# Optimization experiments

Hardware: AMD Instinct MI355X
Metric: run time of the kernel (lower is better)

The kernel has to match this reference:

```python
import jax, jax.numpy as jnp
import numpy as np

N = 400000   # nnum_t (tokens)
C = 256      # dim
H = 8        # num_heads
HD = C // H  # head_dim = 32
K = 32       # patch_size
D = 4        # dilation
BLOCK = K * D
NA = ((N + BLOCK - 1) // BLOCK) * BLOCK  # nnum_a (padded length)
SCALE = HD ** -0.5
INVALID = -1000.0


def setup_inputs() -> dict:
    key = jax.random.key(0)
    ks = jax.random.split(key, 8)
    data = jax.random.normal(ks[0], (N, C), dtype=jnp.float32)
    xyz = jax.random.uniform(ks[1], (N, 3), dtype=jnp.float32) * 1024.0
    depth_idx = jnp.sort(jax.random.randint(ks[2], (N,), 0, 8)).astype(jnp.int64)
    Wqkv = jax.random.normal(ks[3], (C, 3 * C), dtype=jnp.float32) * 0.02
    bqkv = jnp.zeros((3 * C,), dtype=jnp.float32)
    Wproj = jax.random.normal(ks[4], (C, C), dtype=jnp.float32) * 0.02
    bproj = jnp.zeros((C,), dtype=jnp.float32)
    freqs = jax.random.normal(ks[5], (H, HD // 2, 3), dtype=jnp.float32) * 0.02
    return {"data": data, "xyz": xyz, "depth_idx": depth_idx,
            "Wqkv": Wqkv, "bqkv": bqkv, "Wproj": Wproj, "bproj": bproj,
            "freqs": freqs}


def _rotate_half(x):
    x1, x2 = jnp.split(x, 2, axis=-1)
    return jnp.concatenate([-x2, x1], axis=-1)


def reference(data, xyz, depth_idx, Wqkv, bqkv, Wproj, bproj, freqs):
    # qkv projection: (N, 3C)
    qkv = data @ Wqkv + bqkv
    qkv = qkv.reshape(N, 3, H, HD)

    # mixed RoPE: per-head learnable frequencies over 3D positions
    theta = jnp.einsum('nd,hfd->nhf', xyz, freqs)          # (N, H, HD/2)
    emb = jnp.concatenate([theta, theta], axis=-1)         # (N, H, HD)
    cos, sin = jnp.cos(emb), jnp.sin(emb)
    q = qkv[:, 0] * cos + _rotate_half(qkv[:, 0]) * sin
    k = qkv[:, 1] * cos + _rotate_half(qkv[:, 1]) * sin
    v = qkv[:, 2]
    qkv = jnp.stack([q, k, v], axis=1).reshape(N, 3 * C)

    # patch_partition: pad tokens to nnum_a
    pad = NA - N
    qkv = jnp.pad(qkv, ((0, pad), (0, 0)))
    max_d = depth_idx.max()
    depth_p = jnp.pad(depth_idx, (0, pad), constant_values=0) 
    if pad > 0:
        depth_p = depth_p.at[N:].set(max_d + 1)

    # dilation reshuffle: (-1, K, D, 3C) -> (-1, D, K, 3C) -> (-1, K, 3C)
    qkv = qkv.reshape(-1, K, D, 3 * C).transpose(0, 2, 1, 3).reshape(-1, K, 3 * C)
    # split heads: (B, H, K, HD) each
    qkv = qkv.reshape(-1, K, 3, H, HD).transpose(2, 0, 3, 1, 4)
    q, k, v = qkv[0], qkv[1], qkv[2]

    # teacher-forcing mask from depth indices (dilated layout, cond='le')
    m = depth_p.reshape(-1, K, D).transpose(0, 2, 1).reshape(-1, K)  # (B, K)
    diff = m[:, :, None] - m[:, None, :]
    mask = jnp.where(diff < 0, INVALID, 0.0).astype(jnp.float32)     # (B, K, K)

    # windowed attention
    scores = jnp.einsum('bhqd,bhkd->bhqk', q, k) * SCALE + mask[:, None]
    attn = jax.nn.softmax(scores, axis=-1)
    out = jnp.einsum('bhqk,bhkd->bhqd', attn, v)           # (B, H, K, HD)
    out = out.transpose(0, 2, 1, 3).reshape(-1, C)

    # reverse dilation reshuffle and unpad
    out = out.reshape(-1, D, K, C).transpose(0, 2, 1, 3).reshape(-1, C)
    out = out[:N]

    # output projection (dropout is identity at p=0 / eval)
    return out @ Wproj + bproj
```

## Files before the change

kernel.cpp:

```cpp
#include <hip/hip_runtime.h>
#include <math.h>


typedef float  float4v __attribute__((ext_vector_type(4)));
typedef short  bf16x8  __attribute__((ext_vector_type(8)));
typedef unsigned short us4 __attribute__((ext_vector_type(4)));

#define SCALE_ 0.17677669529663687f
#define INV2PI 0.15915494309189535f

__device__ __forceinline__ unsigned short f2bf(float x) {
  union { float f; unsigned u; } v; v.f = x;
  unsigned r = v.u + 0x7FFFu + ((v.u >> 16) & 1u);
  return (unsigned short)(r >> 16);
}
__device__ __forceinline__ unsigned pack2bf(float lo, float hi) {
  return (unsigned)f2bf(lo) | ((unsigned)f2bf(hi) << 16);
}
__device__ __forceinline__ float4v mfma16(bf16x8 a, bf16x8 b, float4v c) {
  return __builtin_amdgcn_mfma_f32_16x16x32_bf16(a, b, c, 0, 0, 0);
}
__device__ __forceinline__ int swz(int off) {
  return off ^ (((off >> 9) & 7) << 4);
}

__global__ __launch_bounds__(256) void k_prep(const float* __restrict__ wqkv,
                                              const float* __restrict__ wproj,
                                              unsigned short* __restrict__ wq,
                                              unsigned short* __restrict__ wp) {
  int tid = blockIdx.x * 256 + threadIdx.x;
  if (tid < 768 * 256) {
    int co = tid >> 8, ci = tid & 255;
    wq[tid] = f2bf(wqkv[ci * 768 + co]);
  } else {
    int u = tid - 768 * 256;
    int co = u >> 8, cpos = u & 255;
    int h = cpos >> 5, ww = cpos & 31;
    int f = (ww & 1) ? 16 + (ww >> 1) : (ww >> 1);
    wp[u] = f2bf(wproj[(h * 32 + f) * 256 + co]);
  }
}

#define K1_LDS_BYTES 81920

__global__ __launch_bounds__(512, 4) void k_fused(
    const float* __restrict__ data, const float* __restrict__ xyz,
    const int* __restrict__ depth, const float* __restrict__ bqkv,
    const float* __restrict__ freqs, const unsigned short* __restrict__ wqkv_t,
    unsigned short* __restrict__ aout ) {
  extern __shared__ char smem[];
  const int b    = blockIdx.x;
  const int t    = threadIdx.x;
  const int lane = t & 63;
  const int w    = t >> 6;
  const int g    = lane >> 4;
  const int l15  = lane & 15;
  const int d    = w >> 1;
  const int half = w & 1;

  if (t < 128) ((int*)(smem + 78336))[t] =
      depth[b * 128 + ((t & 31) << 2) + (t >> 5)];
  if (t < 384) ((float*)(smem + 78848))[t] = xyz[(size_t)b * 384 + t];
  if (t < 384) ((float*)(smem + 80384))[t] = freqs[t];

  {
    const float* dbase = data + (size_t)b * 32768;
#pragma unroll
    for (int i = 0; i < 16; ++i) {
      const int fidx = i * 512 + t;
      const float4v v4 = *reinterpret_cast<const float4v*>(dbase + fidx * 4);
      us4 pk;
      pk.x = f2bf(v4.x); pk.y = f2bf(v4.y); pk.z = f2bf(v4.z); pk.w = f2bf(v4.w);
      *reinterpret_cast<us4*>(smem + swz(fidx * 8)) = pk;
    }
  }
  __syncthreads();

  bf16x8 areg[8];
#pragma unroll
  for (int s = 0; s < 8; ++s)
    areg[s] = *reinterpret_cast<const bf16x8*>(
        smem + swz((16 * w + l15) * 512 + s * 64 + g * 16));

  const int* ML = (const int*)(smem + 78336);
  int mq[4];
#pragma unroll
  for (int rr = 0; rr < 4; ++rr) mq[rr] = ML[32 * d + 16 * half + 4 * g + rr];
  const int mk0 = ML[32 * d + l15];
  const int mk1 = ML[32 * d + 16 + l15];
  __syncthreads();

#pragma unroll 1
  for (int h = 0; h < 8; ++h) {
    {
      const char* wb = (const char*)(wqkv_t) + (size_t)h * 32 * 512;
      bf16x8 s0, s1, s2, s3, s4, s5;
      s0 = *reinterpret_cast<const bf16x8*>(wb + t * 16);
      s1 = *reinterpret_cast<const bf16x8*>(wb + 8192 + t * 16);
      s2 = *reinterpret_cast<const bf16x8*>(wb + 131072 + t * 16);
      s3 = *reinterpret_cast<const bf16x8*>(wb + 131072 + 8192 + t * 16);
      s4 = *reinterpret_cast<const bf16x8*>(wb + 262144 + t * 16);
      s5 = *reinterpret_cast<const bf16x8*>(wb + 262144 + 8192 + t * 16);
      const int o0 = swz(t * 16), o1 = swz(8192 + t * 16);
      *reinterpret_cast<bf16x8*>(smem + o0) = s0;
      *reinterpret_cast<bf16x8*>(smem + o1) = s1;
      *reinterpret_cast<bf16x8*>(smem + 16384 + o0) = s2;
      *reinterpret_cast<bf16x8*>(smem + 16384 + o1) = s3;
      *reinterpret_cast<bf16x8*>(smem + 32768 + o0) = s4;
      *reinterpret_cast<bf16x8*>(smem + 32768 + o1) = s5;
    }
    __syncthreads();

    {
      float4v aq0 = {0.f,0.f,0.f,0.f}, aq1 = aq0, ak0 = aq0, ak1 = aq0;
#pragma unroll
      for (int s = 0; s < 8; ++s) {
        const int ko = s * 64 + g * 16;
        bf16x8 bq0 = *reinterpret_cast<const bf16x8*>(smem + swz(l15 * 512 + ko));
        bf16x8 bq1 = *reinterpret_cast<const bf16x8*>(smem + swz((l15 + 16) * 512 + ko));
        bf16x8 bk0 = *reinterpret_cast<const bf16x8*>(smem + 16384 + swz(l15 * 512 + ko));
        bf16x8 bk1 = *reinterpret_cast<const bf16x8*>(smem + 16384 + swz((l15 + 16) * 512 + ko));
        aq0 = mfma16(areg[s], bq0, aq0);
        aq1 = mfma16(areg[s], bq1, aq1);
        ak0 = mfma16(areg[s], bk0, ak0);
        ak1 = mfma16(areg[s], bk1, ak1);
      }
      const float bq0v = bqkv[h * 32 + l15];
      const float bq1v = bqkv[h * 32 + 16 + l15];
      const float bk0v = bqkv[256 + h * 32 + l15];
      const float bk1v = bqkv[256 + h * 32 + 16 + l15];
      const float* Fp = (const float*)(smem + 80384) + (h * 16 + l15) * 3;
      const float F0 = Fp[0], F1 = Fp[1], F2 = Fp[2];
#pragma unroll
      for (int rr = 0; rr < 4; ++rr) {
        const int row = 16 * w + 4 * g + rr;
        const float* xp = (const float*)(smem + 78848) + row * 3;
        const float th = xp[0] * F0 + xp[1] * F1 + xp[2] * F2;
        float rev = th * INV2PI;
        rev -= floorf(rev);
        const float sn = __builtin_amdgcn_sinf(rev);
        const float cs = __builtin_amdgcn_cosf(rev);
        const int prow = ((row & 3) << 5) | (row >> 2);
        const float q0 = aq0[rr] + bq0v, q1 = aq1[rr] + bq1v;
        const float k0 = ak0[rr] + bk0v, k1 = ak1[rr] + bk1v;
        *reinterpret_cast<unsigned*>(smem + 49152 + prow * 80 + 4 * l15) =
            pack2bf(q0 * cs - q1 * sn, q1 * cs + q0 * sn);
        *reinterpret_cast<unsigned*>(smem + 59392 + prow * 80 + 4 * l15) =
            pack2bf(k0 * cs - k1 * sn, k1 * cs + k0 * sn);
      }
    }
    {
      float4v av0 = {0.f,0.f,0.f,0.f}, av1 = av0;
#pragma unroll
      for (int s = 0; s < 8; ++s) {
        const int ko = s * 64 + g * 16;
        bf16x8 bv0 = *reinterpret_cast<const bf16x8*>(smem + 32768 + swz(l15 * 512 + ko));
        bf16x8 bv1 = *reinterpret_cast<const bf16x8*>(smem + 32768 + swz((l15 + 16) * 512 + ko));
        av0 = mfma16(areg[s], bv0, av0);
        av1 = mfma16(areg[s], bv1, av1);
      }
      const float bv0v = bqkv[512 + h * 32 + l15];
      const float bv1v = bqkv[512 + h * 32 + 16 + l15];
#pragma unroll
      for (int rr = 0; rr < 4; ++rr) {
        const int row = 16 * w + 4 * g + rr;
        const int kk = row >> 2, dd = row & 3;
        const int cpos = (kk < 16) ? (kk << 1) : (((kk - 16) << 1) | 1);
        *reinterpret_cast<unsigned short*>(
            smem + 69632 + l15 * 272 + (dd * 32 + cpos) * 2) = f2bf(av0[rr] + bv0v);
        *reinterpret_cast<unsigned short*>(
            smem + 69632 + (l15 + 16) * 272 + (dd * 32 + cpos) * 2) = f2bf(av1[rr] + bv1v);
      }
    }
    __syncthreads();

    {
      const bf16x8 aq = *reinterpret_cast<const bf16x8*>(
          smem + 49152 + (32 * d + 16 * half + l15) * 80 + 16 * g);
      const bf16x8 bk0 = *reinterpret_cast<const bf16x8*>(
          smem + 59392 + (32 * d + l15) * 80 + 16 * g);
      const bf16x8 bk1 = *reinterpret_cast<const bf16x8*>(
          smem + 59392 + (32 * d + 16 + l15) * 80 + 16 * g);
      float4v s0 = {0.f,0.f,0.f,0.f}, s1 = s0;
      s0 = mfma16(aq, bk0, s0);
      s1 = mfma16(aq, bk1, s1);

      char* plw = smem + w * 1280;
      float rs[4];
#pragma unroll
      for (int rr = 0; rr < 4; ++rr) {
        const float sv0 = s0[rr] * SCALE_ + (mq[rr] < mk0 ? -1000.f : 0.f);
        const float sv1 = s1[rr] * SCALE_ + (mq[rr] < mk1 ? -1000.f : 0.f);
        const float p0 = __expf(sv0);
        const float p1 = __expf(sv1);
        float sm = p0 + p1;
        sm += __shfl_xor(sm, 1);
        sm += __shfl_xor(sm, 2);
        sm += __shfl_xor(sm, 4);
        sm += __shfl_xor(sm, 8);
        rs[rr] = 1.0f / sm;
        *reinterpret_cast<unsigned*>(plw + (4 * g + rr) * 80 + 4 * l15) =
            pack2bf(p0, p1);
      }
      const bf16x8 ap = *reinterpret_cast<const bf16x8*>(plw + l15 * 80 + 16 * g);
      const bf16x8 bv0 = *reinterpret_cast<const bf16x8*>(
          smem + 69632 + l15 * 272 + d * 64 + 16 * g);
      const bf16x8 bv1 = *reinterpret_cast<const bf16x8*>(
          smem + 69632 + (l15 + 16) * 272 + d * 64 + 16 * g);
      float4v o0 = {0.f,0.f,0.f,0.f}, o1 = o0;
      o0 = mfma16(ap, bv0, o0);
      o1 = mfma16(ap, bv1, o1);

      char* ob = (char*)aout + (size_t)b * 131072 + h * 64;
#pragma unroll
      for (int rr = 0; rr < 4; ++rr) {
        const int n_local = (16 * half + 4 * g + rr) * 4 + d;
        *reinterpret_cast<unsigned*>(ob + n_local * 512 + 4 * l15) =
            pack2bf(o0[rr] * rs[rr], o1[rr] * rs[rr]);
      }
    }
    __syncthreads();
  }
}

#define K2_LDS_BYTES 81920

__global__ __launch_bounds__(512, 4) void k_proj(
    const unsigned short* ain,
    const unsigned short* __restrict__ wproj_t,
    const float* __restrict__ bproj,
    float* out) {
  extern __shared__ char smem[];
  const int b = blockIdx.x, t = threadIdx.x;
  const int lane = t & 63, w = t >> 6;
  const int g = lane >> 4, l15 = lane & 15;

  {
    const char* abase = (const char*)ain + (size_t)b * 131072;
    bf16x8 stg[8];
#pragma unroll
    for (int i = 0; i < 8; ++i)
      stg[i] = *reinterpret_cast<const bf16x8*>(abase + i * 8192 + t * 16);
#pragma unroll
    for (int i = 0; i < 8; ++i)
      *reinterpret_cast<bf16x8*>(smem + swz(i * 8192 + t * 16)) = stg[i];
  }
  __syncthreads();

  bf16x8 areg[8];
#pragma unroll
  for (int s = 0; s < 8; ++s)
    areg[s] = *reinterpret_cast<const bf16x8*>(
        smem + swz((16 * w + l15) * 512 + s * 64 + g * 16));

#pragma unroll 1
  for (int p = 0; p < 8; ++p) {
    const char* wb = (const char*)wproj_t + p * 16384;
    const bf16x8 s0 = *reinterpret_cast<const bf16x8*>(wb + t * 16);
    const bf16x8 s1 = *reinterpret_cast<const bf16x8*>(wb + 8192 + t * 16);
    __syncthreads();
    *reinterpret_cast<bf16x8*>(smem + 65536 + swz(t * 16)) = s0;
    *reinterpret_cast<bf16x8*>(smem + 65536 + swz(8192 + t * 16)) = s1;
    __syncthreads();

    float4v acc0 = {0.f,0.f,0.f,0.f}, acc1 = acc0;
#pragma unroll
    for (int s = 0; s < 8; ++s) {
      const int ko = s * 64 + g * 16;
      bf16x8 b0 = *reinterpret_cast<const bf16x8*>(smem + 65536 + swz(l15 * 512 + ko));
      bf16x8 b1 = *reinterpret_cast<const bf16x8*>(smem + 65536 + swz((l15 + 16) * 512 + ko));
      acc0 = mfma16(areg[s], b0, acc0);
      acc1 = mfma16(areg[s], b1, acc1);
    }
    const int col0 = 32 * p + l15, col1 = col0 + 16;
    const float bb0 = bproj[col0], bb1 = bproj[col1];
#pragma unroll
    for (int rr = 0; rr < 4; ++rr) {
      const int row = 16 * w + 4 * g + rr;
      out[((size_t)b * 128 + row) * 256 + col0] = acc0[rr] + bb0;
      out[((size_t)b * 128 + row) * 256 + col1] = acc1[rr] + bb1;
    }
  }
}

extern "C" void kernel_launch(void* const* d_in, const int* in_sizes, int n_in,
                              void* d_out, int out_size, void* d_ws, size_t ws_size,
                              hipStream_t stream) {
  const float* data  = (const float*)d_in[0];
  const float* xyz   = (const float*)d_in[1];
  const int*   depth = (const int*)d_in[2];
  const float* wqkv  = (const float*)d_in[3];
  const float* bqkv  = (const float*)d_in[4];
  const float* wproj = (const float*)d_in[5];
  const float* bproj = (const float*)d_in[6];
  const float* freqs = (const float*)d_in[7];

  unsigned short* wqkv_t  = (unsigned short*)d_ws;
  unsigned short* wproj_t = wqkv_t + 768 * 256;

  (void)hipFuncSetAttribute(reinterpret_cast<const void*>(k_fused),
                            hipFuncAttributeMaxDynamicSharedMemorySize, K1_LDS_BYTES);
  (void)hipFuncSetAttribute(reinterpret_cast<const void*>(k_proj),
                            hipFuncAttributeMaxDynamicSharedMemorySize, K2_LDS_BYTES);

  k_prep<<<dim3(1024), dim3(256), 0, stream>>>(wqkv, wproj, wqkv_t, wproj_t);
  k_fused<<<dim3(3125), dim3(512), K1_LDS_BYTES, stream>>>(
      data, xyz, depth, bqkv, freqs, wqkv_t, (unsigned short*)d_out);
  k_proj<<<dim3(3125), dim3(512), K2_LDS_BYTES, stream>>>(
      (const unsigned short*)d_out, wproj_t, bproj, (float*)d_out);
}
```

Measured before the change: 524.2 us.

## Pre-swizzle QKV weights into MFMA fragment order and compute softmax sum via MFMA

```diff
diff --git a/kernel.cpp b/kernel.cpp
--- a/kernel.cpp
+++ b/kernel.cpp
@@ -26,18 +26,24 @@
 
 __global__ __launch_bounds__(256) void k_prep(const float* __restrict__ wqkv,
                                               const float* __restrict__ wproj,
-                                              unsigned short* __restrict__ wq,
+                                              unsigned short* __restrict__ wqf,
                                               unsigned short* __restrict__ wp) {
   int tid = blockIdx.x * 256 + threadIdx.x;
   if (tid < 768 * 256) {
-    int co = tid >> 8, ci = tid & 255;
-    wq[tid] = f2bf(wqkv[ci * 768 + co]);
+    int h  = tid / 24576;
+    int r  = tid - h * 24576;
+    int mat = r >> 13;
+    int r2  = r & 8191;
+    int s = r2 >> 10, g = (r2 >> 8) & 3, col = (r2 >> 3) & 31, e = r2 & 7;
+    int ci = s * 32 + g * 8 + e;
+    int co = mat * 256 + h * 32 + col;
+    wqf[tid] = f2bf(wqkv[ci * 768 + co]);
   } else {
     int u = tid - 768 * 256;
     int co = u >> 8, cpos = u & 255;
-    int h = cpos >> 5, ww = cpos & 31;
+    int hh = cpos >> 5, ww = cpos & 31;
     int f = (ww & 1) ? 16 + (ww >> 1) : (ww >> 1);
-    wp[u] = f2bf(wproj[(h * 32 + f) * 256 + co]);
+    wp[u] = f2bf(wproj[(hh * 32 + f) * 256 + co]);
   }
 }
 
@@ -46,7 +52,7 @@
 __global__ __launch_bounds__(512, 4) void k_fused(
     const float* __restrict__ data, const float* __restrict__ xyz,
     const int* __restrict__ depth, const float* __restrict__ bqkv,
-    const float* __restrict__ freqs, const unsigned short* __restrict__ wqkv_t,
+    const float* __restrict__ freqs, const unsigned short* __restrict__ wqf,
     unsigned short* __restrict__ aout ) {
   extern __shared__ char smem[];
   const int b    = blockIdx.x;
@@ -82,48 +88,58 @@
     areg[s] = *reinterpret_cast<const bf16x8*>(
         smem + swz((16 * w + l15) * 512 + s * 64 + g * 16));
 
-  const int* ML = (const int*)(smem + 78336);
-  int mq[4];
-#pragma unroll
-  for (int rr = 0; rr < 4; ++rr) mq[rr] = ML[32 * d + 16 * half + 4 * g + rr];
-  const int mk0 = ML[32 * d + l15];
-  const int mk1 = ML[32 * d + 16 + l15];
+  float maskf0[4], maskf1[4];
+  {
+    const int* ML = (const int*)(smem + 78336);
+    const int mk0 = ML[32 * d + l15];
+    const int mk1 = ML[32 * d + 16 + l15];
+#pragma unroll
+    for (int rr = 0; rr < 4; ++rr) {
+      const int mq = ML[32 * d + 16 * half + 4 * g + rr];
+      maskf0[rr] = (mq < mk0) ? -1000.f : 0.f;
+      maskf1[rr] = (mq < mk1) ? -1000.f : 0.f;
+    }
+  }
+  bf16x8 ones;
+#pragma unroll
+  for (int j = 0; j < 8; ++j) ones[j] = (short)0x3F80;
+
   __syncthreads();
+
+  const int bb = g * 512 + l15 * 16;
 
 #pragma unroll 1
   for (int h = 0; h < 8; ++h) {
     {
-      const char* wb = (const char*)(wqkv_t) + (size_t)h * 32 * 512;
-      bf16x8 s0, s1, s2, s3, s4, s5;
-      s0 = *reinterpret_cast<const bf16x8*>(wb + t * 16);
-      s1 = *reinterpret_cast<const bf16x8*>(wb + 8192 + t * 16);
-      s2 = *reinterpret_cast<const bf16x8*>(wb + 131072 + t * 16);
-      s3 = *reinterpret_cast<const bf16x8*>(wb + 131072 + 8192 + t * 16);
-      s4 = *reinterpret_cast<const bf16x8*>(wb + 262144 + t * 16);
-      s5 = *reinterpret_cast<const bf16x8*>(wb + 262144 + 8192 + t * 16);
-      const int o0 = swz(t * 16), o1 = swz(8192 + t * 16);
-      *reinterpret_cast<bf16x8*>(smem + o0) = s0;
-      *reinterpret_cast<bf16x8*>(smem + o1) = s1;
-      *reinterpret_cast<bf16x8*>(smem + 16384 + o0) = s2;
-      *reinterpret_cast<bf16x8*>(smem + 16384 + o1) = s3;
-      *reinterpret_cast<bf16x8*>(smem + 32768 + o0) = s4;
-      *reinterpret_cast<bf16x8*>(smem + 32768 + o1) = s5;
+      const char* wb = (const char*)wqf + (size_t)h * 49152 + t * 16;
+      const bf16x8 s0 = *reinterpret_cast<const bf16x8*>(wb);
+      const bf16x8 s1 = *reinterpret_cast<const bf16x8*>(wb + 8192);
+      const bf16x8 s2 = *reinterpret_cast<const bf16x8*>(wb + 16384);
+      const bf16x8 s3 = *reinterpret_cast<const bf16x8*>(wb + 24576);
+      const bf16x8 s4 = *reinterpret_cast<const bf16x8*>(wb + 32768);
+      const bf16x8 s5 = *reinterpret_cast<const bf16x8*>(wb + 40960);
+      char* wd = smem + t * 16;
+      *reinterpret_cast<bf16x8*>(wd)         = s0;
+      *reinterpret_cast<bf16x8*>(wd + 8192)  = s1;
+      *reinterpret_cast<bf16x8*>(wd + 16384) = s2;
+      *reinterpret_cast<bf16x8*>(wd + 24576) = s3;
+      *reinterpret_cast<bf16x8*>(wd + 32768) = s4;
+      *reinterpret_cast<bf16x8*>(wd + 40960) = s5;
     }
     __syncthreads();
 
     {
-      float4v aq0 = {0.f,0.f,0.f,0.f}, aq1 = aq0, ak0 = aq0, ak1 = aq0;
+      float4v q0a = {0.f,0.f,0.f,0.f}, q1a = q0a, k0a = q0a, k1a = q0a;
 #pragma unroll
       for (int s = 0; s < 8; ++s) {
-        const int ko = s * 64 + g * 16;
-        bf16x8 bq0 = *reinterpret_cast<const bf16x8*>(smem + swz(l15 * 512 + ko));
-        bf16x8 bq1 = *reinterpret_cast<const bf16x8*>(smem + swz((l15 + 16) * 512 + ko));
-        bf16x8 bk0 = *reinterpret_cast<const bf16x8*>(smem + 16384 + swz(l15 * 512 + ko));
-        bf16x8 bk1 = *reinterpret_cast<const bf16x8*>(smem + 16384 + swz((l15 + 16) * 512 + ko));
-        aq0 = mfma16(areg[s], bq0, aq0);
-        aq1 = mfma16(areg[s], bq1, aq1);
-        ak0 = mfma16(areg[s], bk0, ak0);
-        ak1 = mfma16(areg[s], bk1, ak1);
+        const bf16x8 bq0 = *reinterpret_cast<const bf16x8*>(smem + bb + s * 2048);
+        const bf16x8 bq1 = *reinterpret_cast<const bf16x8*>(smem + bb + s * 2048 + 256);
+        const bf16x8 bk0 = *reinterpret_cast<const bf16x8*>(smem + bb + s * 2048 + 16384);
+        const bf16x8 bk1 = *reinterpret_cast<const bf16x8*>(smem + bb + s * 2048 + 16384 + 256);
+        q0a = mfma16(areg[s], bq0, q0a);
+        q1a = mfma16(areg[s], bq1, q1a);
+        k0a = mfma16(areg[s], bk0, k0a);
+        k1a = mfma16(areg[s], bk1, k1a);
       }
       const float bq0v = bqkv[h * 32 + l15];
       const float bq1v = bqkv[h * 32 + 16 + l15];
@@ -133,16 +149,16 @@
       const float F0 = Fp[0], F1 = Fp[1], F2 = Fp[2];
 #pragma unroll
       for (int rr = 0; rr < 4; ++rr) {
-        const int row = 16 * w + 4 * g + rr;
+        const int row  = 16 * w + 4 * g + rr;
+        const int prow = ((row & 3) << 5) | (row >> 2);
         const float* xp = (const float*)(smem + 78848) + row * 3;
         const float th = xp[0] * F0 + xp[1] * F1 + xp[2] * F2;
         float rev = th * INV2PI;
         rev -= floorf(rev);
         const float sn = __builtin_amdgcn_sinf(rev);
         const float cs = __builtin_amdgcn_cosf(rev);
-        const int prow = ((row & 3) << 5) | (row >> 2);
-        const float q0 = aq0[rr] + bq0v, q1 = aq1[rr] + bq1v;
-        const float k0 = ak0[rr] + bk0v, k1 = ak1[rr] + bk1v;
+        const float q0 = q0a[rr] + bq0v, q1 = q1a[rr] + bq1v;
+        const float k0 = k0a[rr] + bk0v, k1 = k1a[rr] + bk1v;
         *reinterpret_cast<unsigned*>(smem + 49152 + prow * 80 + 4 * l15) =
             pack2bf(q0 * cs - q1 * sn, q1 * cs + q0 * sn);
         *reinterpret_cast<unsigned*>(smem + 59392 + prow * 80 + 4 * l15) =
@@ -150,14 +166,13 @@
       }
     }
     {
-      float4v av0 = {0.f,0.f,0.f,0.f}, av1 = av0;
+      float4v v0a = {0.f,0.f,0.f,0.f}, v1a = v0a;
 #pragma unroll
       for (int s = 0; s < 8; ++s) {
-        const int ko = s * 64 + g * 16;
-        bf16x8 bv0 = *reinterpret_cast<const bf16x8*>(smem + 32768 + swz(l15 * 512 + ko));
-        bf16x8 bv1 = *reinterpret_cast<const bf16x8*>(smem + 32768 + swz((l15 + 16) * 512 + ko));
-        av0 = mfma16(areg[s], bv0, av0);
-        av1 = mfma16(areg[s], bv1, av1);
+        const bf16x8 bv0 = *reinterpret_cast<const bf16x8*>(smem + bb + s * 2048 + 32768);
+        const bf16x8 bv1 = *reinterpret_cast<const bf16x8*>(smem + bb + s * 2048 + 32768 + 256);
+        v0a = mfma16(areg[s], bv0, v0a);
+        v1a = mfma16(areg[s], bv1, v1a);
       }
       const float bv0v = bqkv[512 + h * 32 + l15];
       const float bv1v = bqkv[512 + h * 32 + 16 + l15];
@@ -167,9 +182,9 @@
         const int kk = row >> 2, dd = row & 3;
         const int cpos = (kk < 16) ? (kk << 1) : (((kk - 16) << 1) | 1);
         *reinterpret_cast<unsigned short*>(
-            smem + 69632 + l15 * 272 + (dd * 32 + cpos) * 2) = f2bf(av0[rr] + bv0v);
+            smem + 69632 + l15 * 272 + (dd * 32 + cpos) * 2) = f2bf(v0a[rr] + bv0v);
         *reinterpret_cast<unsigned short*>(
-            smem + 69632 + (l15 + 16) * 272 + (dd * 32 + cpos) * 2) = f2bf(av1[rr] + bv1v);
+            smem + 69632 + (l15 + 16) * 272 + (dd * 32 + cpos) * 2) = f2bf(v1a[rr] + bv1v);
       }
     }
     __syncthreads();
@@ -186,19 +201,10 @@
       s1 = mfma16(aq, bk1, s1);
 
       char* plw = smem + w * 1280;
-      float rs[4];
 #pragma unroll
       for (int rr = 0; rr < 4; ++rr) {
-        const float sv0 = s0[rr] * SCALE_ + (mq[rr] < mk0 ? -1000.f : 0.f);
-        const float sv1 = s1[rr] * SCALE_ + (mq[rr] < mk1 ? -1000.f : 0.f);
-        const float p0 = __expf(sv0);
-        const float p1 = __expf(sv1);
-        float sm = p0 + p1;
-        sm += __shfl_xor(sm, 1);
-        sm += __shfl_xor(sm, 2);
-        sm += __shfl_xor(sm, 4);
-        sm += __shfl_xor(sm, 8);
-        rs[rr] = 1.0f / sm;
+        const float p0 = __expf(s0[rr] * SCALE_ + maskf0[rr]);
+        const float p1 = __expf(s1[rr] * SCALE_ + maskf1[rr]);
         *reinterpret_cast<unsigned*>(plw + (4 * g + rr) * 80 + 4 * l15) =
             pack2bf(p0, p1);
       }
@@ -207,16 +213,18 @@
           smem + 69632 + l15 * 272 + d * 64 + 16 * g);
       const bf16x8 bv1 = *reinterpret_cast<const bf16x8*>(
           smem + 69632 + (l15 + 16) * 272 + d * 64 + 16 * g);
-      float4v o0 = {0.f,0.f,0.f,0.f}, o1 = o0;
-      o0 = mfma16(ap, bv0, o0);
-      o1 = mfma16(ap, bv1, o1);
+      float4v o0 = {0.f,0.f,0.f,0.f}, o1 = o0, osum = o0;
+      osum = mfma16(ap, ones, osum);
+      o0   = mfma16(ap, bv0, o0);
+      o1   = mfma16(ap, bv1, o1);
 
       char* ob = (char*)aout + (size_t)b * 131072 + h * 64;
 #pragma unroll
       for (int rr = 0; rr < 4; ++rr) {
+        const float rs = __builtin_amdgcn_rcpf(osum[rr]);
         const int n_local = (16 * half + 4 * g + rr) * 4 + d;
         *reinterpret_cast<unsigned*>(ob + n_local * 512 + 4 * l15) =
-            pack2bf(o0[rr] * rs[rr], o1[rr] * rs[rr]);
+            pack2bf(o0[rr] * rs, o1[rr] * rs);
       }
     }
     __syncthreads();
@@ -230,7 +238,7 @@
     const unsigned short* __restrict__ wproj_t,
     const float* __restrict__ bproj,
     float* out) {
-  extern __shared__ char smem[];
+  extern __shared__ char smem2[];
   const int b = blockIdx.x, t = threadIdx.x;
   const int lane = t & 63, w = t >> 6;
   const int g = lane >> 4, l15 = lane & 15;
@@ -243,7 +251,7 @@
       stg[i] = *reinterpret_cast<const bf16x8*>(abase + i * 8192 + t * 16);
 #pragma unroll
     for (int i = 0; i < 8; ++i)
-      *reinterpret_cast<bf16x8*>(smem + swz(i * 8192 + t * 16)) = stg[i];
+      *reinterpret_cast<bf16x8*>(smem2 + swz(i * 8192 + t * 16)) = stg[i];
   }
   __syncthreads();
 
@@ -251,7 +259,7 @@
 #pragma unroll
   for (int s = 0; s < 8; ++s)
     areg[s] = *reinterpret_cast<const bf16x8*>(
-        smem + swz((16 * w + l15) * 512 + s * 64 + g * 16));
+        smem2 + swz((16 * w + l15) * 512 + s * 64 + g * 16));
 
 #pragma unroll 1
   for (int p = 0; p < 8; ++p) {
@@ -259,16 +267,16 @@
     const bf16x8 s0 = *reinterpret_cast<const bf16x8*>(wb + t * 16);
     const bf16x8 s1 = *reinterpret_cast<const bf16x8*>(wb + 8192 + t * 16);
     __syncthreads();
-    *reinterpret_cast<bf16x8*>(smem + 65536 + swz(t * 16)) = s0;
-    *reinterpret_cast<bf16x8*>(smem + 65536 + swz(8192 + t * 16)) = s1;
+    *reinterpret_cast<bf16x8*>(smem2 + 65536 + swz(t * 16)) = s0;
+    *reinterpret_cast<bf16x8*>(smem2 + 65536 + swz(8192 + t * 16)) = s1;
     __syncthreads();
 
     float4v acc0 = {0.f,0.f,0.f,0.f}, acc1 = acc0;
 #pragma unroll
     for (int s = 0; s < 8; ++s) {
       const int ko = s * 64 + g * 16;
-      bf16x8 b0 = *reinterpret_cast<const bf16x8*>(smem + 65536 + swz(l15 * 512 + ko));
-      bf16x8 b1 = *reinterpret_cast<const bf16x8*>(smem + 65536 + swz((l15 + 16) * 512 + ko));
+      bf16x8 b0 = *reinterpret_cast<const bf16x8*>(smem2 + 65536 + swz(l15 * 512 + ko));
+      bf16x8 b1 = *reinterpret_cast<const bf16x8*>(smem2 + 65536 + swz((l15 + 16) * 512 + ko));
       acc0 = mfma16(areg[s], b0, acc0);
       acc1 = mfma16(areg[s], b1, acc1);
     }
@@ -295,17 +303,17 @@
   const float* bproj = (const float*)d_in[6];
   const float* freqs = (const float*)d_in[7];
 
-  unsigned short* wqkv_t  = (unsigned short*)d_ws;
-  unsigned short* wproj_t = wqkv_t + 768 * 256;
+  unsigned short* wqkv_f  = (unsigned short*)d_ws;
+  unsigned short* wproj_t = wqkv_f + 768 * 256;
 
   (void)hipFuncSetAttribute(reinterpret_cast<const void*>(k_fused),
                             hipFuncAttributeMaxDynamicSharedMemorySize, K1_LDS_BYTES);
   (void)hipFuncSetAttribute(reinterpret_cast<const void*>(k_proj),
                             hipFuncAttributeMaxDynamicSharedMemorySize, K2_LDS_BYTES);
 
-  k_prep<<<dim3(1024), dim3(256), 0, stream>>>(wqkv, wproj, wqkv_t, wproj_t);
+  k_prep<<<dim3(1024), dim3(256), 0, stream>>>(wqkv, wproj, wqkv_f, wproj_t);
   k_fused<<<dim3(3125), dim3(512), K1_LDS_BYTES, stream>>>(
-      data, xyz, depth, bqkv, freqs, wqkv_t, (unsigned short*)d_out);
+      data, xyz, depth, bqkv, freqs, wqkv_f, (unsigned short*)d_out);
   k_proj<<<dim3(3125), dim3(512), K2_LDS_BYTES, stream>>>(
       (const unsigned short*)d_out, wproj_t, bproj, (float*)d_out);
 }
```

Result: faster. 467.0 us (-10.9%).
